# Kernel optimization log

Hardware: AMD Instinct MI355X
Metric: run time of the kernel (lower is better)

Reference implementation:

```python
import jax, jax.numpy as jnp
import numpy as np

N = 50000      # nodes
E = 800000     # edges
F_NODE = 64    # num_node_features
F_EDGE = 16    # num_edge_features
C = 64         # out_channels
L = 3          # n_hidden_layers
G = 512        # num graphs in batch
NCLS = 10      # num_classes
EPS = 1e-5


def _lin_init(k, shape, fan_in):
    lim = 1.0 / np.sqrt(fan_in)
    return jax.random.uniform(k, shape, jnp.float32, -lim, lim)


def setup_inputs() -> dict:
    key = jax.random.key(0)
    ks = jax.random.split(key, 32)
    inp = {
        "x": jax.random.normal(ks[0], (N, F_NODE), jnp.float32),
        "edge_index": jax.random.randint(ks[1], (2, E), 0, N, jnp.int32),
        "batch": ((jnp.arange(N) * G) // N).astype(jnp.int32),  # sorted, covers all graphs
        "dropout": 0,
        "edge_attr": jax.random.uniform(ks[2], (E, F_EDGE), jnp.float32),
        # conv1: PDNConv(F_NODE, C, F_EDGE, F_EDGE). torch Linear layout [out,in].
        "c1_lw": _lin_init(ks[3], (C, F_NODE), F_NODE),
        "c1_w1": _lin_init(ks[4], (F_EDGE, F_EDGE), F_EDGE),
        "c1_b1": _lin_init(ks[5], (F_EDGE,), F_EDGE),
        "c1_w2": _lin_init(ks[6], (1, F_EDGE), F_EDGE),
        "c1_b2": _lin_init(ks[7], (1,), F_EDGE),
        # hidden_conv_1 / hidden_conv_2: L stacked PDNConv(C, C, F_EDGE, F_EDGE)
        "h1_lw": _lin_init(ks[8], (L, C, C), C),
        "h1_w1": _lin_init(ks[9], (L, F_EDGE, F_EDGE), F_EDGE),
        "h1_b1": _lin_init(ks[10], (L, F_EDGE), F_EDGE),
        "h1_w2": _lin_init(ks[11], (L, 1, F_EDGE), F_EDGE),
        "h1_b2": _lin_init(ks[12], (L, 1), F_EDGE),
        "h2_lw": _lin_init(ks[13], (L, C, C), C),
        "h2_w1": _lin_init(ks[14], (L, F_EDGE, F_EDGE), F_EDGE),
        "h2_b1": _lin_init(ks[15], (L, F_EDGE), F_EDGE),
        "h2_w2": _lin_init(ks[16], (L, 1, F_EDGE), F_EDGE),
        "h2_b2": _lin_init(ks[17], (L, 1), F_EDGE),
        # final classifier Linear(C, NCLS)
        "lin_w": _lin_init(ks[18], (NCLS, C), C),
        "lin_b": _lin_init(ks[19], (NCLS,), C),
    }
    return inp


def _pdn_conv(x, row, col, loop, edge_attr, lw, w1, b1, w2, b2):
    """PDNConv: edge-MLP weight -> add self loops -> gcn_norm -> gather-scale-scatter."""
    # edge weight MLP: Linear -> ReLU -> Linear -> Sigmoid, squeeze to [E]
    w = jax.nn.sigmoid(jnp.squeeze(jax.nn.relu(edge_attr @ w1.T + b1) @ w2.T + b2, -1))
    wf = jnp.concatenate([w, jnp.ones((x.shape[0],), x.dtype)])  # self-loop weight 1
    r = jnp.concatenate([row, loop])
    c = jnp.concatenate([col, loop])
    deg = jax.ops.segment_sum(wf, c, num_segments=x.shape[0])
    dis = jnp.where(deg > 0, 1.0 / jnp.sqrt(deg), 0.0)
    norm = dis[r] * wf * dis[c]                 # gcn_norm edge coefficients
    xl = x @ lw.T                                # node transform [N, C]
    msg = xl[r] * norm[:, None]                  # gather + scale [E+N, C]
    return jax.ops.segment_sum(msg, c, num_segments=x.shape[0])


def _batch_norm(x):
    # fresh BatchNorm each forward: weight=1, bias=0, training-mode batch stats
    mu = jnp.mean(x, axis=0)
    var = jnp.mean(jnp.square(x - mu), axis=0)  # biased var
    return (x - mu) * jax.lax.rsqrt(var + EPS)


def reference(x, edge_index, batch, dropout, edge_attr,
              c1_lw, c1_w1, c1_b1, c1_w2, c1_b2,
              h1_lw, h1_w1, h1_b1, h1_w2, h1_b2,
              h2_lw, h2_w1, h2_b1, h2_w2, h2_b2,
              lin_w, lin_b):
    row, col = edge_index[0], edge_index[1]
    loop = jnp.arange(x.shape[0], dtype=row.dtype)

    x = _pdn_conv(x, row, col, loop, edge_attr, c1_lw, c1_w1, c1_b1, c1_w2, c1_b2)
    x0 = x
    for i in range(L):
        x = jax.nn.relu(_batch_norm(x))
        x = _pdn_conv(x, row, col, loop, edge_attr,
                      h1_lw[i], h1_w1[i], h1_b1[i], h1_w2[i], h1_b2[i])
    x1 = x + x0
    x = x + x0
    for i in range(L):
        x = jax.nn.relu(_batch_norm(x))
        x = _pdn_conv(x, row, col, loop, edge_attr,
                      h2_lw[i], h2_w1[i], h2_b1[i], h2_w2[i], h2_b2[i])
    x2 = jax.nn.relu(x + x0 + x1)
    pooled = jax.ops.segment_max(x2, batch, num_segments=G)  # global max pool [G, C]
    # dropout p passed in is 0 / eval -> identity
    return pooled @ lin_w.T + lin_b
```

## Files before the change

### kernel.cpp

```cpp
#include <hip/hip_runtime.h>
#include <hip/hip_bf16.h>
#include <math.h>

#define NN 50000
#define NE 800000
#define FE 16
#define CC 64
#define NG 512
#define NCLS 10
#define NCONV 7
#define SCAN_B 49

typedef float v2f __attribute__((ext_vector_type(2)));

struct MlpP { const float* w1; const float* b1; const float* w2; const float* b2; };
struct MlpAll { MlpP p[NCONV]; };

__global__ __launch_bounds__(256) void k_hist(const int* __restrict__ ecol, int* __restrict__ cnt) {
  int e = blockIdx.x * 256 + threadIdx.x;
  if (e < NE) atomicAdd(&cnt[ecol[e]], 1);
}

__global__ __launch_bounds__(1024) void k_scanA(const int* __restrict__ cnt, int* __restrict__ excl,
                                                int* __restrict__ bsum) {
  __shared__ int sc[1024];
  int t = threadIdx.x;
  int i = blockIdx.x * 1024 + t;
  int v = (i < NN) ? cnt[i] : 0;
  sc[t] = v;
  __syncthreads();
  for (int off = 1; off < 1024; off <<= 1) {
    int u = (t >= off) ? sc[t - off] : 0;
    __syncthreads();
    sc[t] += u;
    __syncthreads();
  }
  if (i < NN) excl[i] = sc[t] - v;
  if (t == 1023) bsum[blockIdx.x] = sc[1023];
}

__global__ void k_scanB(const int* __restrict__ bsum, int* __restrict__ boff) {
  int lane = threadIdx.x;
  int v = (lane < SCAN_B) ? bsum[lane] : 0;
  int own = v;
  for (int off = 1; off < 64; off <<= 1) {
    int u = __shfl_up(v, off);
    if (lane >= off) v += u;
  }
  if (lane < SCAN_B) boff[lane] = v - own;
}

__global__ __launch_bounds__(1024) void k_scanC(const int* __restrict__ excl, const int* __restrict__ boff,
                                                int* __restrict__ cptr, int* __restrict__ cursor) {
  int i = blockIdx.x * 1024 + threadIdx.x;
  if (i < NN) {
    int p = excl[i] + boff[blockIdx.x];
    cptr[i] = p;
    cursor[i] = p;
  }
  if (i == 0) cptr[NN] = NE;
}

__global__ __launch_bounds__(256) void k_scatter(
    const int* __restrict__ erow, const int* __restrict__ ecol,
    int* __restrict__ cursor, int* __restrict__ csrc, int* __restrict__ pos) {
  int e = blockIdx.x * 256 + threadIdx.x;
  if (e >= NE) return;
  int c = ecol[e];
  int p = atomicAdd(&cursor[c], 1);
  csrc[p] = erow[e];
  pos[e] = p;
}

__global__ __launch_bounds__(256) void k_mlp(
    const int* __restrict__ pos, const float* __restrict__ ea,
    float* __restrict__ wcsr8, MlpAll mw) {
  int ep = blockIdx.x * 256 + threadIdx.x;
  if (ep >= NE / 2) return;
  int e0 = ep * 2;
  const float4* eaA = reinterpret_cast<const float4*>(ea + (size_t)e0 * 16);
  const float4* eaB = reinterpret_cast<const float4*>(ea + (size_t)(e0 + 1) * 16);
  float4 A0 = eaA[0], A1 = eaA[1], A2 = eaA[2], A3 = eaA[3];
  float4 B0 = eaB[0], B1 = eaB[1], B2 = eaB[2], B3 = eaB[3];
  v2f a2[16];
  a2[0]  = (v2f){A0.x, B0.x}; a2[1]  = (v2f){A0.y, B0.y}; a2[2]  = (v2f){A0.z, B0.z}; a2[3]  = (v2f){A0.w, B0.w};
  a2[4]  = (v2f){A1.x, B1.x}; a2[5]  = (v2f){A1.y, B1.y}; a2[6]  = (v2f){A1.z, B1.z}; a2[7]  = (v2f){A1.w, B1.w};
  a2[8]  = (v2f){A2.x, B2.x}; a2[9]  = (v2f){A2.y, B2.y}; a2[10] = (v2f){A2.z, B2.z}; a2[11] = (v2f){A2.w, B2.w};
  a2[12] = (v2f){A3.x, B3.x}; a2[13] = (v2f){A3.y, B3.y}; a2[14] = (v2f){A3.z, B3.z}; a2[15] = (v2f){A3.w, B3.w};
  int2 pp = *reinterpret_cast<const int2*>(pos + e0);
  float wv0[NCONV], wv1[NCONV];
  #pragma unroll
  for (int j = 0; j < NCONV; ++j) {
    const float* w1 = mw.p[j].w1;
    const float* b1 = mw.p[j].b1;
    const float* w2 = mw.p[j].w2;
    float b2v = mw.p[j].b2[0];
    v2f z = {b2v, b2v};
    #pragma unroll
    for (int k = 0; k < 16; ++k) {
      float bk = b1[k];
      float wk = w2[k];
      v2f h = {bk, bk};
      #pragma unroll
      for (int m = 0; m < 16; ++m) {
        h += a2[m] * w1[k * 16 + m];
      }
      h.x = h.x > 0.f ? h.x : 0.f;
      h.y = h.y > 0.f ? h.y : 0.f;
      z += h * wk;
    }
    wv0[j] = 1.f / (1.f + __expf(-z.x));
    wv1[j] = 1.f / (1.f + __expf(-z.y));
  }
  float4* d0 = reinterpret_cast<float4*>(wcsr8 + (size_t)pp.x * 8);
  d0[0] = make_float4(wv0[0], wv0[1], wv0[2], wv0[3]);
  d0[1] = make_float4(wv0[4], wv0[5], wv0[6], 0.f);
  float4* d1 = reinterpret_cast<float4*>(wcsr8 + (size_t)pp.y * 8);
  d1[0] = make_float4(wv1[0], wv1[1], wv1[2], wv1[3]);
  d1[1] = make_float4(wv1[4], wv1[5], wv1[6], 0.f);
}

__global__ __launch_bounds__(256) void k_repack(const float* __restrict__ wcsr8, float* __restrict__ wpl) {
  int p = blockIdx.x * 256 + threadIdx.x;
  if (p >= NE) return;
  const float4* q = reinterpret_cast<const float4*>(wcsr8 + (size_t)p * 8);
  float4 a = q[0], b = q[1];
  wpl[0 * (size_t)NE + p] = a.x;
  wpl[1 * (size_t)NE + p] = a.y;
  wpl[2 * (size_t)NE + p] = a.z;
  wpl[3 * (size_t)NE + p] = a.w;
  wpl[4 * (size_t)NE + p] = b.x;
  wpl[5 * (size_t)NE + p] = b.y;
  wpl[6 * (size_t)NE + p] = b.z;
}

__global__ __launch_bounds__(256) void k_deg(const float* __restrict__ wcsr8,
                                             const int* __restrict__ cptr,
                                             float* __restrict__ dis) {
  int n = blockIdx.x * 256 + threadIdx.x;
  if (n >= NN) return;
  int lo = cptr[n], hi = cptr[n + 1];
  float s0=0,s1=0,s2=0,s3=0,s4=0,s5=0,s6=0;
  for (int k = lo; k < hi; ++k) {
    const float4* q = reinterpret_cast<const float4*>(wcsr8 + (size_t)k * 8);
    float4 a = q[0], b = q[1];
    s0+=a.x; s1+=a.y; s2+=a.z; s3+=a.w; s4+=b.x; s5+=b.y; s6+=b.z;
  }
  dis[0*NN+n]=rsqrtf(s0+1.f); dis[1*NN+n]=rsqrtf(s1+1.f); dis[2*NN+n]=rsqrtf(s2+1.f);
  dis[3*NN+n]=rsqrtf(s3+1.f); dis[4*NN+n]=rsqrtf(s4+1.f); dis[5*NN+n]=rsqrtf(s5+1.f);
  dis[6*NN+n]=rsqrtf(s6+1.f);
}

__global__ __launch_bounds__(256) void k_lwt(const float* __restrict__ c1, const float* __restrict__ h1,
                                             const float* __restrict__ h2, float* __restrict__ lwT) {
  int id = blockIdx.x * 256 + threadIdx.x;
  if (id >= NCONV * CC * CC) return;
  int j = id >> 12;
  int r = id & 4095;
  int co = r >> 6, ci = r & 63;
  const float* src = (j == 0) ? c1 : (j <= 3 ? h1 + (j - 1) * 4096 : h2 + (j - 4) * 4096);
  lwT[j * 4096 + ci * 64 + co] = src[co * 64 + ci];
}

__global__ __launch_bounds__(256) void k_bnstat(const float* __restrict__ src, float* __restrict__ accum) {
  __shared__ float sS[256], sQ[256];
  int t = threadIdx.x;
  int c = t & 63, rg = t >> 6;
  int base = blockIdx.x * 196;
  float S = 0.f, Q = 0.f;
  for (int rr = rg; rr < 196; rr += 4) {
    int r = base + rr;
    if (r < NN) { float v = src[r * 64 + c]; S += v; Q += v * v; }
  }
  sS[t] = S; sQ[t] = Q;
  __syncthreads();
  if (t < 128) { sS[t] += sS[t + 128]; sQ[t] += sQ[t + 128]; }
  __syncthreads();
  if (t < 64) {
    atomicAdd(&accum[c], sS[t] + sS[t + 64]);
    atomicAdd(&accum[64 + c], sQ[t] + sQ[t + 64]);
  }
}

__global__ __launch_bounds__(256) void k_gemm(const float* __restrict__ src, const float* __restrict__ lwT,
                                              const float* __restrict__ accum, const float* __restrict__ dis,
                                              float* __restrict__ dst, int useBN) {
  __shared__ float xs[64 * 65];
  int t = threadIdx.x;
  int rows0 = blockIdx.x * 64;
  for (int i = 0; i < 4; ++i) {
    int f = t + i * 256;
    int r = f >> 4, c4 = (f & 15) * 4;
    int row = rows0 + r;
    float4 v = make_float4(0.f, 0.f, 0.f, 0.f);
    if (row < NN) v = *reinterpret_cast<const float4*>(src + (size_t)row * 64 + c4);
    if (useBN) {
      float4 S = *reinterpret_cast<const float4*>(accum + c4);
      float4 Q = *reinterpret_cast<const float4*>(accum + 64 + c4);
      float mu, var, rs;
      mu = S.x * (1.0f/NN); var = Q.x*(1.0f/NN)-mu*mu; var = var<0.f?0.f:var; rs = rsqrtf(var+1e-5f);
      v.x = (v.x-mu)*rs; v.x = v.x>0.f?v.x:0.f;
      mu = S.y * (1.0f/NN); var = Q.y*(1.0f/NN)-mu*mu; var = var<0.f?0.f:var; rs = rsqrtf(var+1e-5f);
      v.y = (v.y-mu)*rs; v.y = v.y>0.f?v.y:0.f;
      mu = S.z * (1.0f/NN); var = Q.z*(1.0f/NN)-mu*mu; var = var<0.f?0.f:var; rs = rsqrtf(var+1e-5f);
      v.z = (v.z-mu)*rs; v.z = v.z>0.f?v.z:0.f;
      mu = S.w * (1.0f/NN); var = Q.w*(1.0f/NN)-mu*mu; var = var<0.f?0.f:var; rs = rsqrtf(var+1e-5f);
      v.w = (v.w-mu)*rs; v.w = v.w>0.f?v.w:0.f;
    }
    xs[r * 65 + c4 + 0] = v.x;
    xs[r * 65 + c4 + 1] = v.y;
    xs[r * 65 + c4 + 2] = v.z;
    xs[r * 65 + c4 + 3] = v.w;
  }
  __syncthreads();
  int lane = t & 63;
  int cobase = __builtin_amdgcn_readfirstlane((t >> 6) << 4);
  float acc[16];
  #pragma unroll
  for (int u = 0; u < 16; ++u) acc[u] = 0.f;
  #pragma unroll 8
  for (int ci = 0; ci < 64; ++ci) {
    float xv = xs[lane * 65 + ci];
    const float* wrow = lwT + ci * 64 + cobase;
    #pragma unroll
    for (int u = 0; u < 16; ++u) acc[u] += xv * wrow[u];
  }
  __syncthreads();
  int row = rows0 + lane;
  float d = (row < NN) ? dis[row] : 0.f;
  #pragma unroll
  for (int u = 0; u < 16; ++u) xs[lane * 65 + cobase + u] = acc[u] * d;
  __syncthreads();
  for (int i = 0; i < 4; ++i) {
    int f = t + i * 256;
    int r = f >> 4, c4 = (f & 15) * 4;
    int orow = rows0 + r;
    if (orow < NN) {
      float4 v = make_float4(xs[r*65+c4], xs[r*65+c4+1], xs[r*65+c4+2], xs[r*65+c4+3]);
      *reinterpret_cast<float4*>(dst + (size_t)orow * 64 + c4) = v;
    }
  }
}

__global__ __launch_bounds__(256) void k_agg(const float* __restrict__ T, const float* __restrict__ wj,
                                             const int* __restrict__ csrc, const int* __restrict__ cptr,
                                             const float* __restrict__ dis, float* __restrict__ out,
                                             const float* __restrict__ skipA, const float* __restrict__ skipX1,
                                             float* __restrict__ outX1, const int* __restrict__ batch,
                                             int* __restrict__ poolI, int wstride, int mode) {
  int t = threadIdx.x;
  int n = blockIdx.x * 4 + (t >> 6);
  if (n >= NN) return;
  int lane = t & 63;
  int lo = cptr[n], hi = cptr[n + 1];
  float acc = T[(size_t)n * 64 + lane];
  int k = lo;
  for (; k + 8 <= hi; k += 8) {
    int s0=csrc[k+0], s1=csrc[k+1], s2=csrc[k+2], s3=csrc[k+3];
    int s4=csrc[k+4], s5=csrc[k+5], s6=csrc[k+6], s7=csrc[k+7];
    float w0=wj[(size_t)(k+0)*wstride], w1=wj[(size_t)(k+1)*wstride], w2=wj[(size_t)(k+2)*wstride], w3=wj[(size_t)(k+3)*wstride];
    float w4=wj[(size_t)(k+4)*wstride], w5=wj[(size_t)(k+5)*wstride], w6=wj[(size_t)(k+6)*wstride], w7=wj[(size_t)(k+7)*wstride];
    float t0=T[(size_t)s0*64+lane], t1=T[(size_t)s1*64+lane], t2=T[(size_t)s2*64+lane], t3=T[(size_t)s3*64+lane];
    float t4=T[(size_t)s4*64+lane], t5=T[(size_t)s5*64+lane], t6=T[(size_t)s6*64+lane], t7=T[(size_t)s7*64+lane];
    acc += w0*t0; acc += w1*t1; acc += w2*t2; acc += w3*t3;
    acc += w4*t4; acc += w5*t5; acc += w6*t6; acc += w7*t7;
  }
  for (; k + 4 <= hi; k += 4) {
    int s0=csrc[k+0], s1=csrc[k+1], s2=csrc[k+2], s3=csrc[k+3];
    float w0=wj[(size_t)(k+0)*wstride], w1=wj[(size_t)(k+1)*wstride], w2=wj[(size_t)(k+2)*wstride], w3=wj[(size_t)(k+3)*wstride];
    float t0=T[(size_t)s0*64+lane], t1=T[(size_t)s1*64+lane], t2=T[(size_t)s2*64+lane], t3=T[(size_t)s3*64+lane];
    acc += w0*t0; acc += w1*t1; acc += w2*t2; acc += w3*t3;
  }
  for (; k < hi; ++k) {
    int s0 = csrc[k];
    float w0 = wj[(size_t)k * wstride];
    acc += w0 * T[(size_t)s0 * 64 + lane];
  }
  float v = dis[n] * acc;
  size_t idx = (size_t)n * 64 + lane;
  if (mode == 1) {
    outX1[idx] = v + skipA[idx];
  } else if (mode == 2) {
    float sv = v + skipA[idx] + skipX1[idx];
    sv = sv > 0.f ? sv : 0.f;
    int g = batch[n];
    atomicMax(&poolI[(size_t)g * 64 + lane], __float_as_int(sv));
  } else {
    out[idx] = v;
  }
}

__global__ __launch_bounds__(256) void k_cls(const float* __restrict__ pooled, const float* __restrict__ lw,
                                             const float* __restrict__ lb, float* __restrict__ out) {
  int id = blockIdx.x * 256 + threadIdx.x;
  if (id >= NG * NCLS) return;
  int g = id / NCLS, k = id % NCLS;
  float acc = lb[k];
  #pragma unroll 8
  for (int c = 0; c < 64; ++c) acc += pooled[g * 64 + c] * lw[k * 64 + c];
  out[id] = acc;
}

extern "C" void kernel_launch(void* const* d_in, const int* in_sizes, int n_in,
                              void* d_out, int out_size, void* d_ws, size_t ws_size,
                              hipStream_t stream) {
  (void)in_sizes; (void)n_in; (void)out_size;
  const float* x     = (const float*)d_in[0];
  const int*   ei    = (const int*)d_in[1];
  const int*   batch = (const int*)d_in[2];
  const float* ea    = (const float*)d_in[4];
  const float* c1_lw = (const float*)d_in[5];
  const float* c1_w1 = (const float*)d_in[6];
  const float* c1_b1 = (const float*)d_in[7];
  const float* c1_w2 = (const float*)d_in[8];
  const float* c1_b2 = (const float*)d_in[9];
  const float* h1_lw = (const float*)d_in[10];
  const float* h1_w1 = (const float*)d_in[11];
  const float* h1_b1 = (const float*)d_in[12];
  const float* h1_w2 = (const float*)d_in[13];
  const float* h1_b2 = (const float*)d_in[14];
  const float* h2_lw = (const float*)d_in[15];
  const float* h2_w1 = (const float*)d_in[16];
  const float* h2_b1 = (const float*)d_in[17];
  const float* h2_w2 = (const float*)d_in[18];
  const float* h2_b2 = (const float*)d_in[19];
  const float* lin_w = (const float*)d_in[20];
  const float* lin_b = (const float*)d_in[21];
  float* out = (float*)d_out;

  char* base = (char*)d_ws;
  size_t off = 0;
  auto alloc = [&](size_t bytes) -> size_t {
    size_t o = off;
    off = (off + bytes + 255) & ~(size_t)255;
    return o;
  };
  size_t o_wcsr8  = alloc((size_t)NE * 8 * 4);
  size_t o_csrc   = alloc((size_t)NE * 4);
  size_t o_pos    = alloc((size_t)NE * 4);
  size_t o_cptr   = alloc((size_t)(NN + 1) * 4);
  size_t o_excl   = alloc((size_t)NN * 4);
  size_t o_bsum   = alloc((size_t)64 * 4);
  size_t o_boff   = alloc((size_t)64 * 4);
  size_t o_cnt    = alloc((size_t)NN * 4);
  size_t o_accum  = alloc((size_t)6 * 128 * 4);
  size_t o_dis    = alloc((size_t)NCONV * NN * 4);
  size_t o_lwt    = alloc((size_t)NCONV * 4096 * 4);
  size_t o_T      = alloc((size_t)NN * 64 * 4);
  size_t o_A      = alloc((size_t)NN * 64 * 4);
  size_t o_B      = alloc((size_t)NN * 64 * 4);
  size_t o_X1     = alloc((size_t)NN * 64 * 4);
  size_t o_pool   = alloc((size_t)NG * 64 * 4);
  size_t o_wpl    = alloc((size_t)NCONV * NE * 4);
  bool use_planes = (off <= ws_size);

  float* wcsr8  = (float*)(base + o_wcsr8);
  int*   csrc   = (int*)(base + o_csrc);
  int*   pos    = (int*)(base + o_pos);
  int*   cptr   = (int*)(base + o_cptr);
  int*   excl   = (int*)(base + o_excl);
  int*   bsum   = (int*)(base + o_bsum);
  int*   boff   = (int*)(base + o_boff);
  int*   cnt    = (int*)(base + o_cnt);
  float* accum  = (float*)(base + o_accum);
  float* dis    = (float*)(base + o_dis);
  float* lwt    = (float*)(base + o_lwt);
  float* T      = (float*)(base + o_T);
  float* A      = (float*)(base + o_A);
  float* B      = (float*)(base + o_B);
  float* X1     = (float*)(base + o_X1);
  float* pooled = (float*)(base + o_pool);
  float* wpl    = (float*)(base + o_wpl);

  hipMemsetAsync(base + o_cnt, 0, o_dis - o_cnt, stream);
  hipMemsetAsync(base + o_pool, 0, (size_t)NG * 64 * 4, stream);

  const int* erow = ei;
  const int* ecol = ei + NE;

  k_hist<<<(NE + 255) / 256, 256, 0, stream>>>(ecol, cnt);
  k_scanA<<<SCAN_B, 1024, 0, stream>>>(cnt, excl, bsum);
  k_scanB<<<1, 64, 0, stream>>>(bsum, boff);
  k_scanC<<<SCAN_B, 1024, 0, stream>>>(excl, boff, cptr, cnt);
  k_scatter<<<(NE + 255) / 256, 256, 0, stream>>>(erow, ecol, cnt, csrc, pos);

  MlpAll mw;
  mw.p[0] = {c1_w1, c1_b1, c1_w2, c1_b2};
  for (int i = 0; i < 3; ++i) {
    mw.p[1 + i] = {h1_w1 + i * 256, h1_b1 + i * 16, h1_w2 + i * 16, h1_b2 + i};
    mw.p[4 + i] = {h2_w1 + i * 256, h2_b1 + i * 16, h2_w2 + i * 16, h2_b2 + i};
  }
  k_mlp<<<(NE / 2 + 255) / 256, 256, 0, stream>>>(pos, ea, wcsr8, mw);
  if (use_planes) k_repack<<<(NE + 255) / 256, 256, 0, stream>>>(wcsr8, wpl);
  k_deg<<<(NN + 255) / 256, 256, 0, stream>>>(wcsr8, cptr, dis);
  k_lwt<<<(NCONV * 4096) / 256, 256, 0, stream>>>(c1_lw, h1_lw, h2_lw, lwt);

  const int GB = (NN + 63) / 64;
  const int AB = (NN + 3) / 4;
  auto wbase = [&](int j) -> const float* {
    return use_planes ? (wpl + (size_t)j * NE) : (wcsr8 + j);
  };
  const int WS = use_planes ? 1 : 8;

  k_gemm<<<GB, 256, 0, stream>>>(x, lwt, nullptr, dis, T, 0);
  k_agg<<<AB, 256, 0, stream>>>(T, wbase(0), csrc, cptr, dis, A,
                                nullptr, nullptr, nullptr, nullptr, nullptr, WS, 0);

  for (int i = 0; i < 3; ++i) {
    const float* src = (i == 0) ? A : B;
    k_bnstat<<<256, 256, 0, stream>>>(src, accum + i * 128);
    k_gemm<<<GB, 256, 0, stream>>>(src, lwt + (1 + i) * 4096, accum + i * 128,
                                   dis + (size_t)(1 + i) * NN, T, 1);
    int mode = (i == 2) ? 1 : 0;
    k_agg<<<AB, 256, 0, stream>>>(T, wbase(1 + i), csrc, cptr,
                                  dis + (size_t)(1 + i) * NN, B, A, nullptr, X1,
                                  nullptr, nullptr, WS, mode);
  }
  for (int i = 0; i < 3; ++i) {
    const float* src = (i == 0) ? X1 : B;
    k_bnstat<<<256, 256, 0, stream>>>(src, accum + (3 + i) * 128);
    k_gemm<<<GB, 256, 0, stream>>>(src, lwt + (4 + i) * 4096, accum + (3 + i) * 128,
                                   dis + (size_t)(4 + i) * NN, T, 1);
    int mode = (i == 2) ? 2 : 0;
    k_agg<<<AB, 256, 0, stream>>>(T, wbase(4 + i), csrc, cptr,
                                  dis + (size_t)(4 + i) * NN, B, A, X1, nullptr,
                                  batch, (int*)pooled, WS, mode);
  }

  k_cls<<<(NG * NCLS + 255) / 256, 256, 0, stream>>>(pooled, lin_w, lin_b, out);
}
```

Measured before the change: 644.5 us.

## Aggregate four edges per wavefront with float4 gathers; four edges per MLP thread

The aggregation kernel now splits each 64-lane wavefront into four groups of 16 lanes. Each group handles a different edge using float4 row loads, and the partial sums are combined with cross-lane shuffles. The next edge's index and weight are prefetched, and the skip, output and pool writes are vectorised. Separately, the edge-MLP kernel processes four edges per thread so weight loads are shared and more independent FMAs run at once. The cost is higher register pressure in the MLP and reduction overhead for low-degree nodes.

```diff
diff --git a/kernel.cpp b/kernel.cpp
--- a/kernel.cpp
+++ b/kernel.cpp
@@ -76,41 +76,53 @@
     const int* __restrict__ pos, const float* __restrict__ ea,
     float* __restrict__ wcsr8, MlpAll mw) {
   int ep = blockIdx.x * 256 + threadIdx.x;
-  if (ep >= NE / 2) return;
-  int e0 = ep * 2;
-  const float4* eaA = reinterpret_cast<const float4*>(ea + (size_t)e0 * 16);
-  const float4* eaB = reinterpret_cast<const float4*>(ea + (size_t)(e0 + 1) * 16);
-  float4 A0 = eaA[0], A1 = eaA[1], A2 = eaA[2], A3 = eaA[3];
-  float4 B0 = eaB[0], B1 = eaB[1], B2 = eaB[2], B3 = eaB[3];
-  v2f a2[16];
-  a2[0]  = (v2f){A0.x, B0.x}; a2[1]  = (v2f){A0.y, B0.y}; a2[2]  = (v2f){A0.z, B0.z}; a2[3]  = (v2f){A0.w, B0.w};
-  a2[4]  = (v2f){A1.x, B1.x}; a2[5]  = (v2f){A1.y, B1.y}; a2[6]  = (v2f){A1.z, B1.z}; a2[7]  = (v2f){A1.w, B1.w};
-  a2[8]  = (v2f){A2.x, B2.x}; a2[9]  = (v2f){A2.y, B2.y}; a2[10] = (v2f){A2.z, B2.z}; a2[11] = (v2f){A2.w, B2.w};
-  a2[12] = (v2f){A3.x, B3.x}; a2[13] = (v2f){A3.y, B3.y}; a2[14] = (v2f){A3.z, B3.z}; a2[15] = (v2f){A3.w, B3.w};
-  int2 pp = *reinterpret_cast<const int2*>(pos + e0);
-  float wv0[NCONV], wv1[NCONV];
+  if (ep >= NE / 4) return;
+  int e0 = ep * 4;
+  const float4* ea4 = reinterpret_cast<const float4*>(ea + (size_t)e0 * 16);
+  float4 A0 = ea4[0],  A1 = ea4[1],  A2 = ea4[2],  A3 = ea4[3];
+  float4 B0 = ea4[4],  B1 = ea4[5],  B2 = ea4[6],  B3 = ea4[7];
+  float4 C0 = ea4[8],  C1 = ea4[9],  C2 = ea4[10], C3 = ea4[11];
+  float4 D0 = ea4[12], D1 = ea4[13], D2 = ea4[14], D3 = ea4[15];
+  v2f aA[16], aB[16];
+  aA[0]  = (v2f){A0.x, B0.x}; aA[1]  = (v2f){A0.y, B0.y}; aA[2]  = (v2f){A0.z, B0.z}; aA[3]  = (v2f){A0.w, B0.w};
+  aA[4]  = (v2f){A1.x, B1.x}; aA[5]  = (v2f){A1.y, B1.y}; aA[6]  = (v2f){A1.z, B1.z}; aA[7]  = (v2f){A1.w, B1.w};
+  aA[8]  = (v2f){A2.x, B2.x}; aA[9]  = (v2f){A2.y, B2.y}; aA[10] = (v2f){A2.z, B2.z}; aA[11] = (v2f){A2.w, B2.w};
+  aA[12] = (v2f){A3.x, B3.x}; aA[13] = (v2f){A3.y, B3.y}; aA[14] = (v2f){A3.z, B3.z}; aA[15] = (v2f){A3.w, B3.w};
+  aB[0]  = (v2f){C0.x, D0.x}; aB[1]  = (v2f){C0.y, D0.y}; aB[2]  = (v2f){C0.z, D0.z}; aB[3]  = (v2f){C0.w, D0.w};
+  aB[4]  = (v2f){C1.x, D1.x}; aB[5]  = (v2f){C1.y, D1.y}; aB[6]  = (v2f){C1.z, D1.z}; aB[7]  = (v2f){C1.w, D1.w};
+  aB[8]  = (v2f){C2.x, D2.x}; aB[9]  = (v2f){C2.y, D2.y}; aB[10] = (v2f){C2.z, D2.z}; aB[11] = (v2f){C2.w, D2.w};
+  aB[12] = (v2f){C3.x, D3.x}; aB[13] = (v2f){C3.y, D3.y}; aB[14] = (v2f){C3.z, D3.z}; aB[15] = (v2f){C3.w, D3.w};
+  int4 pp = *reinterpret_cast<const int4*>(pos + e0);
+  float wv0[NCONV], wv1[NCONV], wv2[NCONV], wv3[NCONV];
   #pragma unroll
   for (int j = 0; j < NCONV; ++j) {
     const float* w1 = mw.p[j].w1;
     const float* b1 = mw.p[j].b1;
     const float* w2 = mw.p[j].w2;
     float b2v = mw.p[j].b2[0];
-    v2f z = {b2v, b2v};
+    v2f zA = {b2v, b2v}, zB = {b2v, b2v};
     #pragma unroll
     for (int k = 0; k < 16; ++k) {
       float bk = b1[k];
       float wk = w2[k];
-      v2f h = {bk, bk};
+      v2f hA = {bk, bk}, hB = {bk, bk};
       #pragma unroll
       for (int m = 0; m < 16; ++m) {
-        h += a2[m] * w1[k * 16 + m];
+        float wm = w1[k * 16 + m];
+        hA += aA[m] * wm;
+        hB += aB[m] * wm;
       }
-      h.x = h.x > 0.f ? h.x : 0.f;
-      h.y = h.y > 0.f ? h.y : 0.f;
-      z += h * wk;
+      hA.x = hA.x > 0.f ? hA.x : 0.f;
+      hA.y = hA.y > 0.f ? hA.y : 0.f;
+      hB.x = hB.x > 0.f ? hB.x : 0.f;
+      hB.y = hB.y > 0.f ? hB.y : 0.f;
+      zA += hA * wk;
+      zB += hB * wk;
     }
-    wv0[j] = 1.f / (1.f + __expf(-z.x));
-    wv1[j] = 1.f / (1.f + __expf(-z.y));
+    wv0[j] = 1.f / (1.f + __expf(-zA.x));
+    wv1[j] = 1.f / (1.f + __expf(-zA.y));
+    wv2[j] = 1.f / (1.f + __expf(-zB.x));
+    wv3[j] = 1.f / (1.f + __expf(-zB.y));
   }
   float4* d0 = reinterpret_cast<float4*>(wcsr8 + (size_t)pp.x * 8);
   d0[0] = make_float4(wv0[0], wv0[1], wv0[2], wv0[3]);
@@ -118,6 +130,12 @@
   float4* d1 = reinterpret_cast<float4*>(wcsr8 + (size_t)pp.y * 8);
   d1[0] = make_float4(wv1[0], wv1[1], wv1[2], wv1[3]);
   d1[1] = make_float4(wv1[4], wv1[5], wv1[6], 0.f);
+  float4* d2 = reinterpret_cast<float4*>(wcsr8 + (size_t)pp.z * 8);
+  d2[0] = make_float4(wv2[0], wv2[1], wv2[2], wv2[3]);
+  d2[1] = make_float4(wv2[4], wv2[5], wv2[6], 0.f);
+  float4* d3 = reinterpret_cast<float4*>(wcsr8 + (size_t)pp.w * 8);
+  d3[0] = make_float4(wv3[0], wv3[1], wv3[2], wv3[3]);
+  d3[1] = make_float4(wv3[4], wv3[5], wv3[6], 0.f);
 }
 
 __global__ __launch_bounds__(256) void k_repack(const float* __restrict__ wcsr8, float* __restrict__ wpl) {
@@ -252,41 +270,66 @@
   int n = blockIdx.x * 4 + (t >> 6);
   if (n >= NN) return;
   int lane = t & 63;
+  int e4 = lane >> 4;
+  int cq = lane & 15;
   int lo = cptr[n], hi = cptr[n + 1];
-  float acc = T[(size_t)n * 64 + lane];
-  int k = lo;
-  for (; k + 8 <= hi; k += 8) {
-    int s0=csrc[k+0], s1=csrc[k+1], s2=csrc[k+2], s3=csrc[k+3];
-    int s4=csrc[k+4], s5=csrc[k+5], s6=csrc[k+6], s7=csrc[k+7];
-    float w0=wj[(size_t)(k+0)*wstride], w1=wj[(size_t)(k+1)*wstride], w2=wj[(size_t)(k+2)*wstride], w3=wj[(size_t)(k+3)*wstride];
-    float w4=wj[(size_t)(k+4)*wstride], w5=wj[(size_t)(k+5)*wstride], w6=wj[(size_t)(k+6)*wstride], w7=wj[(size_t)(k+7)*wstride];
-    float t0=T[(size_t)s0*64+lane], t1=T[(size_t)s1*64+lane], t2=T[(size_t)s2*64+lane], t3=T[(size_t)s3*64+lane];
-    float t4=T[(size_t)s4*64+lane], t5=T[(size_t)s5*64+lane], t6=T[(size_t)s6*64+lane], t7=T[(size_t)s7*64+lane];
-    acc += w0*t0; acc += w1*t1; acc += w2*t2; acc += w3*t3;
-    acc += w4*t4; acc += w5*t5; acc += w6*t6; acc += w7*t7;
-  }
-  for (; k + 4 <= hi; k += 4) {
-    int s0=csrc[k+0], s1=csrc[k+1], s2=csrc[k+2], s3=csrc[k+3];
-    float w0=wj[(size_t)(k+0)*wstride], w1=wj[(size_t)(k+1)*wstride], w2=wj[(size_t)(k+2)*wstride], w3=wj[(size_t)(k+3)*wstride];
-    float t0=T[(size_t)s0*64+lane], t1=T[(size_t)s1*64+lane], t2=T[(size_t)s2*64+lane], t3=T[(size_t)s3*64+lane];
-    acc += w0*t0; acc += w1*t1; acc += w2*t2; acc += w3*t3;
-  }
-  for (; k < hi; ++k) {
-    int s0 = csrc[k];
-    float w0 = wj[(size_t)k * wstride];
-    acc += w0 * T[(size_t)s0 * 64 + lane];
-  }
-  float v = dis[n] * acc;
-  size_t idx = (size_t)n * 64 + lane;
+
+  float4 tn = reinterpret_cast<const float4*>(T + (size_t)n * 64)[cq];
+  float4 acc;
+  acc.x = e4 == 0 ? tn.x : 0.f;
+  acc.y = e4 == 0 ? tn.y : 0.f;
+  acc.z = e4 == 0 ? tn.z : 0.f;
+  acc.w = e4 == 0 ? tn.w : 0.f;
+
+  int base = lo;
+  int k = base + e4;
+  bool val = k < hi;
+  int s = val ? csrc[k] : n;
+  float w = val ? wj[(size_t)k * wstride] : 0.f;
+  while (base < hi) {
+    int curs = s;
+    float curw = w;
+    base += 4;
+    k = base + e4;
+    bool v2 = k < hi;
+    s = v2 ? csrc[k] : n;
+    w = v2 ? wj[(size_t)k * wstride] : 0.f;
+    float4 q = reinterpret_cast<const float4*>(T + (size_t)curs * 64)[cq];
+    acc.x += curw * q.x;
+    acc.y += curw * q.y;
+    acc.z += curw * q.z;
+    acc.w += curw * q.w;
+  }
+
+  acc.x += __shfl_xor(acc.x, 16); acc.y += __shfl_xor(acc.y, 16);
+  acc.z += __shfl_xor(acc.z, 16); acc.w += __shfl_xor(acc.w, 16);
+  acc.x += __shfl_xor(acc.x, 32); acc.y += __shfl_xor(acc.y, 32);
+  acc.z += __shfl_xor(acc.z, 32); acc.w += __shfl_xor(acc.w, 32);
+
+  if (e4 != 0) return;
+  float d = dis[n];
+  float4 v = make_float4(acc.x * d, acc.y * d, acc.z * d, acc.w * d);
+  size_t ridx = (size_t)n * 16 + cq;
   if (mode == 1) {
-    outX1[idx] = v + skipA[idx];
+    float4 a = reinterpret_cast<const float4*>(skipA)[ridx];
+    float4 sv = make_float4(v.x + a.x, v.y + a.y, v.z + a.z, v.w + a.w);
+    reinterpret_cast<float4*>(outX1)[ridx] = sv;
   } else if (mode == 2) {
-    float sv = v + skipA[idx] + skipX1[idx];
-    sv = sv > 0.f ? sv : 0.f;
+    float4 a = reinterpret_cast<const float4*>(skipA)[ridx];
+    float4 x1 = reinterpret_cast<const float4*>(skipX1)[ridx];
+    float4 sv = make_float4(v.x + a.x + x1.x, v.y + a.y + x1.y, v.z + a.z + x1.z, v.w + a.w + x1.w);
+    sv.x = sv.x > 0.f ? sv.x : 0.f;
+    sv.y = sv.y > 0.f ? sv.y : 0.f;
+    sv.z = sv.z > 0.f ? sv.z : 0.f;
+    sv.w = sv.w > 0.f ? sv.w : 0.f;
     int g = batch[n];
-    atomicMax(&poolI[(size_t)g * 64 + lane], __float_as_int(sv));
+    int* pb = poolI + (size_t)g * 64 + cq * 4;
+    atomicMax(pb + 0, __float_as_int(sv.x));
+    atomicMax(pb + 1, __float_as_int(sv.y));
+    atomicMax(pb + 2, __float_as_int(sv.z));
+    atomicMax(pb + 3, __float_as_int(sv.w));
   } else {
-    out[idx] = v;
+    reinterpret_cast<float4*>(out)[ridx] = v;
   }
 }
 
@@ -390,7 +433,7 @@
     mw.p[1 + i] = {h1_w1 + i * 256, h1_b1 + i * 16, h1_w2 + i * 16, h1_b2 + i};
     mw.p[4 + i] = {h2_w1 + i * 256, h2_b1 + i * 16, h2_w2 + i * 16, h2_b2 + i};
   }
-  k_mlp<<<(NE / 2 + 255) / 256, 256, 0, stream>>>(pos, ea, wcsr8, mw);
+  k_mlp<<<(NE / 4 + 255) / 256, 256, 0, stream>>>(pos, ea, wcsr8, mw);
   if (use_planes) k_repack<<<(NE + 255) / 256, 256, 0, stream>>>(wcsr8, wpl);
   k_deg<<<(NN + 255) / 256, 256, 0, stream>>>(wcsr8, cptr, dis);
   k_lwt<<<(NCONV * 4096) / 256, 256, 0, stream>>>(c1_lw, h1_lw, h2_lw, lwt);
```

Measured after the change: 662.3 us. +2.8%, slower.
